# Kernel tuning notes

Hardware: AMD Instinct MI355X
Metric: run time of the kernel (lower is better)

Reference implementation:

```python
import jax, jax.numpy as jnp
from jax import lax
import numpy as np

SEQ, B, IN, H = 512, 64, 1024, 1024


def setup_inputs() -> dict:
    key = jax.random.key(0)
    ks = jax.random.split(key, 9)
    s = 0.02
    return {
        "x":   jax.random.normal(ks[0], (SEQ, B, IN), dtype=jnp.float32),
        # layer 0: Linear(input_dim, hidden) and Linear(hidden, hidden)
        "Wi0": jax.random.normal(ks[1], (H, IN), dtype=jnp.float32) * s,
        "bi0": jax.random.normal(ks[2], (H,), dtype=jnp.float32) * s,
        "Wh0": jax.random.normal(ks[3], (H, H), dtype=jnp.float32) * s,
        "bh0": jax.random.normal(ks[4], (H,), dtype=jnp.float32) * s,
        # layer 1: Linear(hidden, hidden) twice
        "Wi1": jax.random.normal(ks[5], (H, H), dtype=jnp.float32) * s,
        "bi1": jax.random.normal(ks[6], (H,), dtype=jnp.float32) * s,
        "Wh1": jax.random.normal(ks[7], (H, H), dtype=jnp.float32) * s,
        "bh1": jax.random.normal(ks[8], (H,), dtype=jnp.float32) * s,
    }


def reference(x, Wi0, bi0, Wh0, bh0, Wi1, bi1, Wh1, bh1):
    # x: [seq, batch, in]; two-layer tanh RNN, time-major, zero initial hidden.
    batch = x.shape[1]
    hdim = Wh0.shape[0]
    h0 = jnp.zeros((2, batch, hdim), dtype=x.dtype)

    def step(h_prev, x_t):
        h1 = jnp.tanh(x_t @ Wi0.T + bi0 + h_prev[0] @ Wh0.T + bh0)
        h2 = jnp.tanh(h1 @ Wi1.T + bi1 + h_prev[1] @ Wh1.T + bh1)
        return jnp.stack([h1, h2], axis=0), h2

    h_final, outputs = lax.scan(step, h0, x)
    return outputs, h_final
```

## Files before the change

### kernel.cpp

```cpp
#include <hip/hip_runtime.h>


#define SEQ 512
#define BATCH 64
#define HID 1024
#define BH (BATCH * HID)
#define DEPTH 8

typedef __attribute__((ext_vector_type(8))) short short8;
typedef __attribute__((ext_vector_type(4))) float f32x4;
typedef __attribute__((ext_vector_type(4))) unsigned int u32x4;

__device__ __forceinline__ unsigned short f32_to_bf16_rne(float f) {
    unsigned int u = __float_as_uint(f);
    u += 0x7FFFu + ((u >> 16) & 1u);
    return (unsigned short)(u >> 16);
}

__device__ __forceinline__ short8 cvt8(float4 f0, float4 f1) {
    short8 w;
    w[0] = (short)f32_to_bf16_rne(f0.x);
    w[1] = (short)f32_to_bf16_rne(f0.y);
    w[2] = (short)f32_to_bf16_rne(f0.z);
    w[3] = (short)f32_to_bf16_rne(f0.w);
    w[4] = (short)f32_to_bf16_rne(f1.x);
    w[5] = (short)f32_to_bf16_rne(f1.y);
    w[6] = (short)f32_to_bf16_rne(f1.z);
    w[7] = (short)f32_to_bf16_rne(f1.w);
    return w;
}

__device__ __forceinline__ void ld_cc16(short8& d, const unsigned short* p) {
    asm volatile("global_load_dwordx4 %0, %1, off sc0 sc1"
                 : "=v"(d) : "v"(p) : "memory");
}

__device__ __forceinline__ void vm_wait0() {
    asm volatile("s_waitcnt vmcnt(0)" ::: "memory");
    __builtin_amdgcn_sched_barrier(0);
}

__device__ __forceinline__ void st_cc16(unsigned short* p, unsigned v) {
    asm volatile("global_store_short %0, %1, off sc0 sc1"
                 :: "v"(p), "v"(v) : "memory");
}

__device__ __forceinline__ unsigned min_u16x4(u32x4 w, unsigned mn) {
    #pragma unroll
    for (int j = 0; j < 4; ++j) {
        unsigned lo = w[j] & 0xFFFFu, hi = w[j] >> 16;
        mn = mn < lo ? mn : lo;
        mn = mn < hi ? mn : hi;
    }
    return mn;
}

__device__ __forceinline__ void wait_one32(const unsigned short* f, int target) {
    if (target <= 0) return;
    for (;;) {
        u32x4 r[4];
        #pragma unroll
        for (int i = 0; i < 4; ++i)
            asm volatile("global_load_dwordx4 %0, %1, off sc0 sc1"
                         : "=v"(r[i]) : "v"((const unsigned int*)f + i * 4) : "memory");
        asm volatile("s_waitcnt vmcnt(0)" ::: "memory");
        __builtin_amdgcn_sched_barrier(0);
        unsigned mn = 0xFFFFu;
        #pragma unroll
        for (int i = 0; i < 4; ++i) mn = min_u16x4(r[i], mn);
        if ((int)mn >= target) return;
        __builtin_amdgcn_s_sleep(1);
    }
}

__device__ __forceinline__ void wait_two32(const unsigned short* f0, int t0,
                                           const unsigned short* f1, int t1) {
    if (t0 <= 0 && t1 <= 0) return;
    for (;;) {
        u32x4 r0[4], r1[4];
        #pragma unroll
        for (int i = 0; i < 4; ++i)
            asm volatile("global_load_dwordx4 %0, %1, off sc0 sc1"
                         : "=v"(r0[i]) : "v"((const unsigned int*)f0 + i * 4) : "memory");
        #pragma unroll
        for (int i = 0; i < 4; ++i)
            asm volatile("global_load_dwordx4 %0, %1, off sc0 sc1"
                         : "=v"(r1[i]) : "v"((const unsigned int*)f1 + i * 4) : "memory");
        asm volatile("s_waitcnt vmcnt(0)" ::: "memory");
        __builtin_amdgcn_sched_barrier(0);
        unsigned m0 = 0xFFFFu, m1 = 0xFFFFu;
        #pragma unroll
        for (int i = 0; i < 4; ++i) { m0 = min_u16x4(r0[i], m0); m1 = min_u16x4(r1[i], m1); }
        if ((int)m0 >= t0 && (int)m1 >= t1) return;
        __builtin_amdgcn_s_sleep(1);
    }
}

#define MFMA16(W, A, ACC) \
    ACC = __builtin_amdgcn_mfma_f32_16x16x32_bf16((W), (A), (ACC), 0, 0, 0)

__device__ __forceinline__ void ring_mm16(const unsigned short* pr, size_t aoff,
                                          const short8* wreg, f32x4& acc) {
    short8 a[16];
    #pragma unroll
    for (int k = 0; k < 16; ++k)
        ld_cc16(a[k], pr + aoff + k * 32);
    vm_wait0();
    #pragma unroll
    for (int k = 0; k < 16; ++k)
        MFMA16(wreg[k], a[k], acc);
}

__global__ void cvt_f32_bf16(const float* __restrict__ src,
                             unsigned short* __restrict__ dst, int n4) {
    int i = blockIdx.x * blockDim.x + threadIdx.x;
    int stride = gridDim.x * blockDim.x;
    for (; i < n4; i += stride) {
        float4 f = ((const float4*)src)[i];
        ushort4 o;
        o.x = f32_to_bf16_rne(f.x);
        o.y = f32_to_bf16_rne(f.y);
        o.z = f32_to_bf16_rne(f.z);
        o.w = f32_to_bf16_rne(f.w);
        ((ushort4*)dst)[i] = o;
    }
}

__global__ void init_ws(uint4* __restrict__ p, int n16) {
    int i = blockIdx.x * blockDim.x + threadIdx.x;
    if (i < n16) p[i] = make_uint4(0u, 0u, 0u, 0u);
}

__global__ __launch_bounds__(512, 1) void rnn_mfma(
    const float* __restrict__ x,
    const unsigned short* __restrict__ xb, int use_xb,
    const float* __restrict__ Wi0, const float* __restrict__ bi0,
    const float* __restrict__ Wh0, const float* __restrict__ bh0,
    const float* __restrict__ Wi1, const float* __restrict__ bi1,
    const float* __restrict__ Wh1, const float* __restrict__ bh1,
    float* __restrict__ out,
    unsigned short* __restrict__ rings,
    unsigned short* __restrict__ flags)
{
    unsigned short* h1ring = rings;
    unsigned short* h2ring = rings + DEPTH * BH;

    const int tid   = threadIdx.x;
    const int wg    = blockIdx.x;
    const int layer = wg >> 7;
    const int rg4   = (wg >> 5) & 3;
    const int nb32  = wg & 31;
    const int wv    = tid >> 6;
    const int lane  = tid & 63;
    const int fb    = wv >> 2;
    const int srcw  = (wv >> 1) & 1;
    const int kh    = wv & 1;

    unsigned short* gL0 = flags + (0 * 4 + rg4) * 64;
    unsigned short* gL1 = flags + (1 * 4 + rg4) * 64;
    unsigned short* ep_self = (layer ? gL1 : gL0) + nb32;

    const float* Wsel = layer ? (srcw ? Wh1 : Wi1) : (srcw ? Wh0 : Wi0);
    const int f_w = nb32 * 32 + fb * 16 + (lane & 15);
    const int kcb = kh * 512 + (lane >> 4) * 8;
    short8 wreg[16];
    {
        const float* rw = Wsel + (size_t)f_w * HID + kcb;
        #pragma unroll
        for (int ks = 0; ks < 16; ++ks)
            wreg[ks] = cvt8(*(const float4*)(rw + ks * 32),
                            *(const float4*)(rw + ks * 32 + 4));
    }

    const int arow = rg4 * 16 + (lane & 15);
    const size_t aoff = (size_t)arow * HID + kcb;

    const int r_feat = tid & 31;
    const int r_row  = tid >> 5;
    const int gf     = nb32 * 32 + r_feat;
    const int grow   = rg4 * 16 + r_row;
    const float* biv = layer ? bi1 : bi0;
    const float* bhv = layer ? bh1 : bh0;
    const float biasv = biv[gf] + bhv[gf];
    const int rw_base = (r_feat >> 4) * 4;

    __shared__ float red[8][16][17];

    for (int s = 0; s < SEQ; ++s) {
        f32x4 acc = {0.f, 0.f, 0.f, 0.f};

        if (layer == 0 && srcw == 0) {
            if (use_xb) {
                const unsigned short* px = xb + (size_t)s * BH + aoff;
                #pragma unroll
                for (int ks = 0; ks < 16; ++ks) {
                    short8 a = *(const short8*)(px + ks * 32);
                    MFMA16(wreg[ks], a, acc);
                }
            } else {
                const float* px = x + (size_t)s * BH + aoff;
                #pragma unroll
                for (int ks = 0; ks < 16; ++ks) {
                    short8 a = cvt8(*(const float4*)(px + ks * 32),
                                    *(const float4*)(px + ks * 32 + 4));
                    MFMA16(wreg[ks], a, acc);
                }
            }
        } else if (layer == 0) {
            if (lane == 0) wait_two32(gL0, s, gL1, s - (DEPTH - 1));
            ring_mm16(h1ring + (size_t)((s - 1) & (DEPTH - 1)) * BH, aoff, wreg, acc);
        } else if (srcw == 1) {
            if (lane == 0) wait_one32(gL1, s);
            ring_mm16(h2ring + (size_t)((s - 1) & (DEPTH - 1)) * BH, aoff, wreg, acc);
        } else {
            if (lane == 0) wait_one32(gL0, s + 1);
            ring_mm16(h1ring + (size_t)(s & (DEPTH - 1)) * BH, aoff, wreg, acc);
        }

        #pragma unroll
        for (int r = 0; r < 4; ++r)
            red[wv][4 * (lane >> 4) + r][lane & 15] = acc[r];
        __syncthreads();

        float v;
        {
            const int ff = r_feat & 15;
            v = red[rw_base][ff][r_row] + red[rw_base + 1][ff][r_row]
              + red[rw_base + 2][ff][r_row] + red[rw_base + 3][ff][r_row] + biasv;
            v = tanhf(v);
            unsigned short* ring_self =
                (layer ? h2ring : h1ring) + (size_t)(s & (DEPTH - 1)) * BH;
            st_cc16(ring_self + (size_t)grow * HID + gf, f32_to_bf16_rne(v));
        }

        asm volatile("s_waitcnt vmcnt(0)" ::: "memory");
        __builtin_amdgcn_sched_barrier(0);
        __syncthreads();
        if (tid == 0)
            st_cc16(ep_self, (unsigned)(s + 1));

        if (layer == 1) {
            out[(size_t)s * BH + (size_t)grow * HID + gf] = v;
            if (s == SEQ - 1)
                out[(size_t)SEQ * BH + BH + (size_t)grow * HID + gf] = v;
        } else if (s == SEQ - 1) {
            out[(size_t)SEQ * BH + (size_t)grow * HID + gf] = v;
        }
    }
}

extern "C" void kernel_launch(void* const* d_in, const int* in_sizes, int n_in,
                              void* d_out, int out_size, void* d_ws, size_t ws_size,
                              hipStream_t stream) {
    const float* xp   = (const float*)d_in[0];
    const float* Wi0p = (const float*)d_in[1];
    const float* bi0p = (const float*)d_in[2];
    const float* Wh0p = (const float*)d_in[3];
    const float* bh0p = (const float*)d_in[4];
    const float* Wi1p = (const float*)d_in[5];
    const float* bi1p = (const float*)d_in[6];
    const float* Wh1p = (const float*)d_in[7];
    const float* bh1p = (const float*)d_in[8];
    float* outp = (float*)d_out;

    unsigned short* rings = (unsigned short*)d_ws;
    const size_t ring_bytes = (size_t)2 * DEPTH * BH * sizeof(unsigned short);
    unsigned short* flags = (unsigned short*)((char*)d_ws + ring_bytes);
    const size_t flag_pad = 4096;
    unsigned short* xb = (unsigned short*)((char*)d_ws + ring_bytes + flag_pad);
    const size_t xb_bytes = (size_t)SEQ * BH * 2;
    const int use_xb = (ws_size >= ring_bytes + flag_pad + xb_bytes) ? 1 : 0;

    {
        const int n16 = (int)((ring_bytes + flag_pad) / 16);
        init_ws<<<(n16 + 255) / 256, 256, 0, stream>>>((uint4*)d_ws, n16);
    }
    if (use_xb)
        cvt_f32_bf16<<<2048, 256, 0, stream>>>(xp, xb, SEQ * BH / 4);

    rnn_mfma<<<dim3(256), dim3(512), 0, stream>>>(
        xp, xb, use_xb,
        Wi0p, bi0p, Wh0p, bh0p, Wi1p, bi1p, Wh1p, bh1p,
        outp, rings, flags);
}
```

Measured before the change: 3.853 ms.

## Wait only on K-half producer flags and double-buffer flag polling loads

Each wave now polls only the 16 producer flags that cover its half of the K dimension, instead of all 32 flags for the row group. This lets a wave start its ring matmul as soon as the producers it actually reads from are done. The polling loop also keeps one batch of flag loads in flight while it checks the previous batch, which shortens each spin iteration. The write-after-read guard on the layer-1 flags is narrowed to half of the consumers as well. That is a risk, because every layer-1 workgroup reads each layer-0 feature, so a ring slot could be overwritten before some reader has finished with it.

New measurement: 3.949 ms. 1.02x slower.

```diff
diff --git a/kernel.cpp b/kernel.cpp
--- a/kernel.cpp
+++ b/kernel.cpp
@@ -55,45 +55,53 @@
     return mn;
 }
 
-__device__ __forceinline__ void wait_one32(const unsigned short* f, int target) {
+__device__ __forceinline__ void issue_half(u32x4& r0, u32x4& r1,
+                                           const unsigned short* f) {
+    asm volatile("global_load_dwordx4 %0, %1, off sc0 sc1"
+                 : "=v"(r0) : "v"((const unsigned int*)f) : "memory");
+    asm volatile("global_load_dwordx4 %0, %1, off sc0 sc1"
+                 : "=v"(r1) : "v"((const unsigned int*)f + 4) : "memory");
+}
+
+__device__ __forceinline__ void wait_half(const unsigned short* f, int target) {
     if (target <= 0) return;
+    u32x4 a0, a1, b0, b1;
+    issue_half(a0, a1, f);
     for (;;) {
-        u32x4 r[4];
-        #pragma unroll
-        for (int i = 0; i < 4; ++i)
-            asm volatile("global_load_dwordx4 %0, %1, off sc0 sc1"
-                         : "=v"(r[i]) : "v"((const unsigned int*)f + i * 4) : "memory");
-        asm volatile("s_waitcnt vmcnt(0)" ::: "memory");
-        __builtin_amdgcn_sched_barrier(0);
-        unsigned mn = 0xFFFFu;
-        #pragma unroll
-        for (int i = 0; i < 4; ++i) mn = min_u16x4(r[i], mn);
-        if ((int)mn >= target) return;
-        __builtin_amdgcn_s_sleep(1);
-    }
-}
-
-__device__ __forceinline__ void wait_two32(const unsigned short* f0, int t0,
+        issue_half(b0, b1, f);
+        asm volatile("s_waitcnt vmcnt(2)" ::: "memory");
+        __builtin_amdgcn_sched_barrier(0);
+        if ((int)min_u16x4(a1, min_u16x4(a0, 0xFFFFu)) >= target) break;
+        __builtin_amdgcn_s_sleep(1);
+        issue_half(a0, a1, f);
+        asm volatile("s_waitcnt vmcnt(2)" ::: "memory");
+        __builtin_amdgcn_sched_barrier(0);
+        if ((int)min_u16x4(b1, min_u16x4(b0, 0xFFFFu)) >= target) break;
+        __builtin_amdgcn_s_sleep(1);
+    }
+    vm_wait0();
+}
+
+__device__ __forceinline__ void wait_half2(const unsigned short* f0, int t0,
                                            const unsigned short* f1, int t1) {
     if (t0 <= 0 && t1 <= 0) return;
+    u32x4 a0, a1, a2, a3, b0, b1, b2, b3;
+    issue_half(a0, a1, f0); issue_half(a2, a3, f1);
     for (;;) {
-        u32x4 r0[4], r1[4];
-        #pragma unroll
-        for (int i = 0; i < 4; ++i)
-            asm volatile("global_load_dwordx4 %0, %1, off sc0 sc1"
-                         : "=v"(r0[i]) : "v"((const unsigned int*)f0 + i * 4) : "memory");
-        #pragma unroll
-        for (int i = 0; i < 4; ++i)
-            asm volatile("global_load_dwordx4 %0, %1, off sc0 sc1"
-                         : "=v"(r1[i]) : "v"((const unsigned int*)f1 + i * 4) : "memory");
-        asm volatile("s_waitcnt vmcnt(0)" ::: "memory");
-        __builtin_amdgcn_sched_barrier(0);
-        unsigned m0 = 0xFFFFu, m1 = 0xFFFFu;
-        #pragma unroll
-        for (int i = 0; i < 4; ++i) { m0 = min_u16x4(r0[i], m0); m1 = min_u16x4(r1[i], m1); }
-        if ((int)m0 >= t0 && (int)m1 >= t1) return;
-        __builtin_amdgcn_s_sleep(1);
-    }
+        issue_half(b0, b1, f0); issue_half(b2, b3, f1);
+        asm volatile("s_waitcnt vmcnt(4)" ::: "memory");
+        __builtin_amdgcn_sched_barrier(0);
+        if ((int)min_u16x4(a1, min_u16x4(a0, 0xFFFFu)) >= t0 &&
+            (int)min_u16x4(a3, min_u16x4(a2, 0xFFFFu)) >= t1) break;
+        __builtin_amdgcn_s_sleep(1);
+        issue_half(a0, a1, f0); issue_half(a2, a3, f1);
+        asm volatile("s_waitcnt vmcnt(4)" ::: "memory");
+        __builtin_amdgcn_sched_barrier(0);
+        if ((int)min_u16x4(b1, min_u16x4(b0, 0xFFFFu)) >= t0 &&
+            (int)min_u16x4(b3, min_u16x4(b2, 0xFFFFu)) >= t1) break;
+        __builtin_amdgcn_s_sleep(1);
+    }
+    vm_wait0();
 }
 
 #define MFMA16(W, A, ACC) \
@@ -159,6 +167,8 @@
     unsigned short* gL0 = flags + (0 * 4 + rg4) * 64;
     unsigned short* gL1 = flags + (1 * 4 + rg4) * 64;
     unsigned short* ep_self = (layer ? gL1 : gL0) + nb32;
+    const unsigned short* dataL0 = gL0 + kh * 16;
+    const unsigned short* dataL1 = gL1 + kh * 16;
 
     const float* Wsel = layer ? (srcw ? Wh1 : Wi1) : (srcw ? Wh0 : Wi0);
     const int f_w = nb32 * 32 + fb * 16 + (lane & 15);
@@ -207,13 +217,13 @@
                 }
             }
         } else if (layer == 0) {
-            if (lane == 0) wait_two32(gL0, s, gL1, s - (DEPTH - 1));
+            if (lane == 0) wait_half2(dataL0, s, dataL1, s - (DEPTH - 1));
             ring_mm16(h1ring + (size_t)((s - 1) & (DEPTH - 1)) * BH, aoff, wreg, acc);
         } else if (srcw == 1) {
-            if (lane == 0) wait_one32(gL1, s);
+            if (lane == 0) wait_half(dataL1, s);
             ring_mm16(h2ring + (size_t)((s - 1) & (DEPTH - 1)) * BH, aoff, wreg, acc);
         } else {
-            if (lane == 0) wait_one32(gL0, s + 1);
+            if (lane == 0) wait_half(dataL0, s + 1);
             ring_mm16(h1ring + (size_t)(s & (DEPTH - 1)) * BH, aoff, wreg, acc);
         }
 
```

## Tag ring entries with step counter to replace flag polling with data polling

Applied to the files above, without the earlier changes.

Each hidden-state ring entry is widened to 32 bits and carries the bf16 value plus the producing step number. Consumers poll the data itself until every tag matches, so the per-step flag round trip before reading is gone. The flag is now written right after the reduction barrier and serves only as ring-slot backpressure. Ring depth drops to 4, and a double-buffered shared reduction array removes the second barrier. The cost is twice the ring traffic, the tag-check work on each poll, and correctness now relies on each 32-bit store being seen atomically.

Result: slower. 11.46 ms (+197.5%).

```diff
diff --git a/kernel.cpp b/kernel.cpp
--- a/kernel.cpp
+++ b/kernel.cpp
@@ -5,7 +5,7 @@
 #define BATCH 64
 #define HID 1024
 #define BH (BATCH * HID)
-#define DEPTH 8
+#define DEPTH 4
 
 typedef __attribute__((ext_vector_type(8))) short short8;
 typedef __attribute__((ext_vector_type(4))) float f32x4;
@@ -30,16 +30,15 @@
     return w;
 }
 
-__device__ __forceinline__ void ld_cc16(short8& d, const unsigned short* p) {
-    asm volatile("global_load_dwordx4 %0, %1, off sc0 sc1"
-                 : "=v"(d) : "v"(p) : "memory");
-}
-
 __device__ __forceinline__ void vm_wait0() {
     asm volatile("s_waitcnt vmcnt(0)" ::: "memory");
     __builtin_amdgcn_sched_barrier(0);
 }
 
+__device__ __forceinline__ void st_cc32(unsigned* p, unsigned v) {
+    asm volatile("global_store_dword %0, %1, off sc0 sc1"
+                 :: "v"(p), "v"(v) : "memory");
+}
 __device__ __forceinline__ void st_cc16(unsigned short* p, unsigned v) {
     asm volatile("global_store_short %0, %1, off sc0 sc1"
                  :: "v"(p), "v"(v) : "memory");
@@ -55,7 +54,7 @@
     return mn;
 }
 
-__device__ __forceinline__ void wait_one32(const unsigned short* f, int target) {
+__device__ __forceinline__ void wait_grp32(const unsigned short* f, int target) {
     if (target <= 0) return;
     for (;;) {
         u32x4 r[4];
@@ -73,42 +72,50 @@
     }
 }
 
-__device__ __forceinline__ void wait_two32(const unsigned short* f0, int t0,
-                                           const unsigned short* f1, int t1) {
-    if (t0 <= 0 && t1 <= 0) return;
-    for (;;) {
-        u32x4 r0[4], r1[4];
-        #pragma unroll
-        for (int i = 0; i < 4; ++i)
-            asm volatile("global_load_dwordx4 %0, %1, off sc0 sc1"
-                         : "=v"(r0[i]) : "v"((const unsigned int*)f0 + i * 4) : "memory");
-        #pragma unroll
-        for (int i = 0; i < 4; ++i)
-            asm volatile("global_load_dwordx4 %0, %1, off sc0 sc1"
-                         : "=v"(r1[i]) : "v"((const unsigned int*)f1 + i * 4) : "memory");
-        asm volatile("s_waitcnt vmcnt(0)" ::: "memory");
-        __builtin_amdgcn_sched_barrier(0);
-        unsigned m0 = 0xFFFFu, m1 = 0xFFFFu;
-        #pragma unroll
-        for (int i = 0; i < 4; ++i) { m0 = min_u16x4(r0[i], m0); m1 = min_u16x4(r1[i], m1); }
-        if ((int)m0 >= t0 && (int)m1 >= t1) return;
-        __builtin_amdgcn_s_sleep(1);
-    }
-}
-
 #define MFMA16(W, A, ACC) \
     ACC = __builtin_amdgcn_mfma_f32_16x16x32_bf16((W), (A), (ACC), 0, 0, 0)
 
-__device__ __forceinline__ void ring_mm16(const unsigned short* pr, size_t aoff,
-                                          const short8* wreg, f32x4& acc) {
-    short8 a[16];
-    #pragma unroll
-    for (int k = 0; k < 16; ++k)
-        ld_cc16(a[k], pr + aoff + k * 32);
+__device__ __forceinline__ bool try_ring_mm(const unsigned* pr, unsigned tag,
+                                            const short8* wreg, f32x4& accio) {
+    u32x4 lo[16], hi[16];
+    #pragma unroll
+    for (int ks = 0; ks < 16; ++ks) {
+        const unsigned* p = pr + ks * 32;
+        asm volatile("global_load_dwordx4 %0, %1, off sc0 sc1"
+                     : "=v"(lo[ks]) : "v"(p) : "memory");
+        asm volatile("global_load_dwordx4 %0, %1, off sc0 sc1"
+                     : "=v"(hi[ks]) : "v"(p + 4) : "memory");
+    }
     vm_wait0();
-    #pragma unroll
-    for (int k = 0; k < 16; ++k)
-        MFMA16(wreg[k], a[k], acc);
+    unsigned d = 0;
+    #pragma unroll
+    for (int ks = 0; ks < 16; ++ks) {
+        #pragma unroll
+        for (int j = 0; j < 4; ++j) {
+            d |= lo[ks][j] ^ tag;
+            d |= hi[ks][j] ^ tag;
+        }
+    }
+    if (!__all((d & 0xFFFFu) == 0u)) return false;
+    f32x4 acc = accio;
+    #pragma unroll
+    for (int ks = 0; ks < 16; ++ks) {
+        u32x4 pk;
+        pk[0] = (lo[ks][0] >> 16) | (lo[ks][1] & 0xFFFF0000u);
+        pk[1] = (lo[ks][2] >> 16) | (lo[ks][3] & 0xFFFF0000u);
+        pk[2] = (hi[ks][0] >> 16) | (hi[ks][1] & 0xFFFF0000u);
+        pk[3] = (hi[ks][2] >> 16) | (hi[ks][3] & 0xFFFF0000u);
+        short8 a = __builtin_bit_cast(short8, pk);
+        MFMA16(wreg[ks], a, acc);
+    }
+    accio = acc;
+    return true;
+}
+
+__device__ __forceinline__ void ring_mm_poll(const unsigned* pr, unsigned tag,
+                                             const short8* wreg, f32x4& acc) {
+    while (!try_ring_mm(pr, tag, wreg, acc))
+        __builtin_amdgcn_s_sleep(1);
 }
 
 __global__ void cvt_f32_bf16(const float* __restrict__ src,
@@ -139,11 +146,11 @@
     const float* __restrict__ Wi1, const float* __restrict__ bi1,
     const float* __restrict__ Wh1, const float* __restrict__ bh1,
     float* __restrict__ out,
-    unsigned short* __restrict__ rings,
+    unsigned* __restrict__ rings32,
     unsigned short* __restrict__ flags)
 {
-    unsigned short* h1ring = rings;
-    unsigned short* h2ring = rings + DEPTH * BH;
+    unsigned* h1r = rings32;
+    unsigned* h2r = rings32 + DEPTH * BH;
 
     const int tid   = threadIdx.x;
     const int wg    = blockIdx.x;
@@ -184,10 +191,20 @@
     const float biasv = biv[gf] + bhv[gf];
     const int rw_base = (r_feat >> 4) * 4;
 
-    __shared__ float red[8][16][17];
+    __shared__ float red[2][8][16][17];
 
     for (int s = 0; s < SEQ; ++s) {
+        const int par = s & 1;
         f32x4 acc = {0.f, 0.f, 0.f, 0.f};
+
+        if (tid == 0) {
+            if (layer == 0) {
+                wait_grp32(gL0, s - (DEPTH - 2));
+                wait_grp32(gL1, s - (DEPTH - 1));
+            } else {
+                wait_grp32(gL1, s - (DEPTH - 2));
+            }
+        }
 
         if (layer == 0 && srcw == 0) {
             if (use_xb) {
@@ -207,44 +224,41 @@
                 }
             }
         } else if (layer == 0) {
-            if (lane == 0) wait_two32(gL0, s, gL1, s - (DEPTH - 1));
-            ring_mm16(h1ring + (size_t)((s - 1) & (DEPTH - 1)) * BH, aoff, wreg, acc);
+            ring_mm_poll(h1r + (size_t)((s - 1) & (DEPTH - 1)) * BH + aoff,
+                         (unsigned)s, wreg, acc);
         } else if (srcw == 1) {
-            if (lane == 0) wait_one32(gL1, s);
-            ring_mm16(h2ring + (size_t)((s - 1) & (DEPTH - 1)) * BH, aoff, wreg, acc);
+            ring_mm_poll(h2r + (size_t)((s - 1) & (DEPTH - 1)) * BH + aoff,
+                         (unsigned)s, wreg, acc);
         } else {
-            if (lane == 0) wait_one32(gL0, s + 1);
-            ring_mm16(h1ring + (size_t)(s & (DEPTH - 1)) * BH, aoff, wreg, acc);
+            ring_mm_poll(h1r + (size_t)(s & (DEPTH - 1)) * BH + aoff,
+                         (unsigned)(s + 1), wreg, acc);
         }
 
         #pragma unroll
         for (int r = 0; r < 4; ++r)
-            red[wv][4 * (lane >> 4) + r][lane & 15] = acc[r];
+            red[par][wv][4 * (lane >> 4) + r][lane & 15] = acc[r];
         __syncthreads();
 
-        float v;
+        if (tid == 0)
+            st_cc16(ep_self, (unsigned)(s + 1));
+
         {
             const int ff = r_feat & 15;
-            v = red[rw_base][ff][r_row] + red[rw_base + 1][ff][r_row]
-              + red[rw_base + 2][ff][r_row] + red[rw_base + 3][ff][r_row] + biasv;
+            float v = red[par][rw_base][ff][r_row] + red[par][rw_base + 1][ff][r_row]
+                    + red[par][rw_base + 2][ff][r_row] + red[par][rw_base + 3][ff][r_row]
+                    + biasv;
             v = tanhf(v);
-            unsigned short* ring_self =
-                (layer ? h2ring : h1ring) + (size_t)(s & (DEPTH - 1)) * BH;
-            st_cc16(ring_self + (size_t)grow * HID + gf, f32_to_bf16_rne(v));
-        }
-
-        asm volatile("s_waitcnt vmcnt(0)" ::: "memory");
-        __builtin_amdgcn_sched_barrier(0);
-        __syncthreads();
-        if (tid == 0)
-            st_cc16(ep_self, (unsigned)(s + 1));
-
-        if (layer == 1) {
-            out[(size_t)s * BH + (size_t)grow * HID + gf] = v;
-            if (s == SEQ - 1)
-                out[(size_t)SEQ * BH + BH + (size_t)grow * HID + gf] = v;
-        } else if (s == SEQ - 1) {
-            out[(size_t)SEQ * BH + (size_t)grow * HID + gf] = v;
+            unsigned tagged = ((unsigned)f32_to_bf16_rne(v) << 16) | (unsigned)(s + 1);
+            unsigned* ring_self = (layer ? h2r : h1r) + (size_t)(s & (DEPTH - 1)) * BH;
+            st_cc32(ring_self + (size_t)grow * HID + gf, tagged);
+
+            if (layer == 1) {
+                out[(size_t)s * BH + (size_t)grow * HID + gf] = v;
+                if (s == SEQ - 1)
+                    out[(size_t)SEQ * BH + BH + (size_t)grow * HID + gf] = v;
+            } else if (s == SEQ - 1) {
+                out[(size_t)SEQ * BH + (size_t)grow * HID + gf] = v;
+            }
         }
     }
 }
@@ -263,8 +277,8 @@
     const float* bh1p = (const float*)d_in[8];
     float* outp = (float*)d_out;
 
-    unsigned short* rings = (unsigned short*)d_ws;
-    const size_t ring_bytes = (size_t)2 * DEPTH * BH * sizeof(unsigned short);
+    unsigned* rings32 = (unsigned*)d_ws;
+    const size_t ring_bytes = (size_t)2 * DEPTH * BH * sizeof(unsigned);
     unsigned short* flags = (unsigned short*)((char*)d_ws + ring_bytes);
     const size_t flag_pad = 4096;
     unsigned short* xb = (unsigned short*)((char*)d_ws + ring_bytes + flag_pad);
@@ -281,5 +295,5 @@
     rnn_mfma<<<dim3(256), dim3(512), 0, stream>>>(
         xp, xb, use_xb,
         Wi0p, bi0p, Wh0p, bh0p, Wi1p, bi1p, Wh1p, bh1p,
-        outp, rings, flags);
-}
+        outp, rings32, flags);
+}
```

## Replace block barriers with per-wave LDS flag handoff and finer global flags

Applied to the files above, without the earlier changes.

Removes both __syncthreads per timestep. Each 16-feature half of the block now reduces independently: three producer waves post partial sums to double-buffered LDS and signal with workgroup-scope atomics, and a fourth wave adds its own partial, applies bias and tanh, writes four packed bf16 values, and publishes a per-half global flag. The global flag array doubles to 64 entries per row group, so consumers poll twice as many flags, and all waves (not only lane 0) now spin on them. This is meant to cut intra-block barrier stalls and let halves progress independently, at the cost of more polling traffic and more complex spin-based synchronization.

Result: slower. 10.34 ms (+168.5%).

```diff
diff --git a/kernel.cpp b/kernel.cpp
--- a/kernel.cpp
+++ b/kernel.cpp
@@ -44,6 +44,17 @@
     asm volatile("global_store_short %0, %1, off sc0 sc1"
                  :: "v"(p), "v"(v) : "memory");
 }
+__device__ __forceinline__ void st_cc64(unsigned short* p, unsigned long long v) {
+    asm volatile("global_store_dwordx2 %0, %1, off sc0 sc1"
+                 :: "v"(p), "v"(v) : "memory");
+}
+
+__device__ __forceinline__ unsigned long long pack4_bf16(float a, float b, float c, float d) {
+    return (unsigned long long)f32_to_bf16_rne(a)
+         | ((unsigned long long)f32_to_bf16_rne(b) << 16)
+         | ((unsigned long long)f32_to_bf16_rne(c) << 32)
+         | ((unsigned long long)f32_to_bf16_rne(d) << 48);
+}
 
 __device__ __forceinline__ unsigned min_u16x4(u32x4 w, unsigned mn) {
     #pragma unroll
@@ -55,42 +66,42 @@
     return mn;
 }
 
-__device__ __forceinline__ void wait_one32(const unsigned short* f, int target) {
+__device__ __forceinline__ void wait_one64(const unsigned short* f, int target) {
     if (target <= 0) return;
     for (;;) {
-        u32x4 r[4];
-        #pragma unroll
-        for (int i = 0; i < 4; ++i)
+        u32x4 r[8];
+        #pragma unroll
+        for (int i = 0; i < 8; ++i)
             asm volatile("global_load_dwordx4 %0, %1, off sc0 sc1"
                          : "=v"(r[i]) : "v"((const unsigned int*)f + i * 4) : "memory");
         asm volatile("s_waitcnt vmcnt(0)" ::: "memory");
         __builtin_amdgcn_sched_barrier(0);
         unsigned mn = 0xFFFFu;
         #pragma unroll
-        for (int i = 0; i < 4; ++i) mn = min_u16x4(r[i], mn);
+        for (int i = 0; i < 8; ++i) mn = min_u16x4(r[i], mn);
         if ((int)mn >= target) return;
         __builtin_amdgcn_s_sleep(1);
     }
 }
 
-__device__ __forceinline__ void wait_two32(const unsigned short* f0, int t0,
+__device__ __forceinline__ void wait_two64(const unsigned short* f0, int t0,
                                            const unsigned short* f1, int t1) {
     if (t0 <= 0 && t1 <= 0) return;
     for (;;) {
-        u32x4 r0[4], r1[4];
-        #pragma unroll
-        for (int i = 0; i < 4; ++i)
+        u32x4 r0[8], r1[8];
+        #pragma unroll
+        for (int i = 0; i < 8; ++i)
             asm volatile("global_load_dwordx4 %0, %1, off sc0 sc1"
                          : "=v"(r0[i]) : "v"((const unsigned int*)f0 + i * 4) : "memory");
         #pragma unroll
-        for (int i = 0; i < 4; ++i)
+        for (int i = 0; i < 8; ++i)
             asm volatile("global_load_dwordx4 %0, %1, off sc0 sc1"
                          : "=v"(r1[i]) : "v"((const unsigned int*)f1 + i * 4) : "memory");
         asm volatile("s_waitcnt vmcnt(0)" ::: "memory");
         __builtin_amdgcn_sched_barrier(0);
         unsigned m0 = 0xFFFFu, m1 = 0xFFFFu;
         #pragma unroll
-        for (int i = 0; i < 4; ++i) { m0 = min_u16x4(r0[i], m0); m1 = min_u16x4(r1[i], m1); }
+        for (int i = 0; i < 8; ++i) { m0 = min_u16x4(r0[i], m0); m1 = min_u16x4(r1[i], m1); }
         if ((int)m0 >= t0 && (int)m1 >= t1) return;
         __builtin_amdgcn_s_sleep(1);
     }
@@ -153,14 +164,14 @@
     const int wv    = tid >> 6;
     const int lane  = tid & 63;
     const int fb    = wv >> 2;
-    const int srcw  = (wv >> 1) & 1;
-    const int kh    = wv & 1;
+    const int r2    = wv & 3;
+    const int kh    = r2 & 1;
 
     unsigned short* gL0 = flags + (0 * 4 + rg4) * 64;
     unsigned short* gL1 = flags + (1 * 4 + rg4) * 64;
-    unsigned short* ep_self = (layer ? gL1 : gL0) + nb32;
-
-    const float* Wsel = layer ? (srcw ? Wh1 : Wi1) : (srcw ? Wh0 : Wi0);
+    unsigned short* ep_self = (layer ? gL1 : gL0) + nb32 * 2 + fb;
+
+    const float* Wsel = layer ? (r2 < 2 ? Wh1 : Wi1) : (r2 < 2 ? Wi0 : Wh0);
     const int f_w = nb32 * 32 + fb * 16 + (lane & 15);
     const int kcb = kh * 512 + (lane >> 4) * 8;
     short8 wreg[16];
@@ -175,21 +186,30 @@
     const int arow = rg4 * 16 + (lane & 15);
     const size_t aoff = (size_t)arow * HID + kcb;
 
-    const int r_feat = tid & 31;
-    const int r_row  = tid >> 5;
-    const int gf     = nb32 * 32 + r_feat;
-    const int grow   = rg4 * 16 + r_row;
+    const int f0   = nb32 * 32 + fb * 16 + 4 * (lane >> 4);
+    const int grow = rg4 * 16 + (lane & 15);
     const float* biv = layer ? bi1 : bi0;
     const float* bhv = layer ? bh1 : bh0;
-    const float biasv = biv[gf] + bhv[gf];
-    const int rw_base = (r_feat >> 4) * 4;
-
-    __shared__ float red[8][16][17];
+    float bias4[4];
+    #pragma unroll
+    for (int r = 0; r < 4; ++r) bias4[r] = biv[f0 + r] + bhv[f0 + r];
+
+    __shared__ float part[2][2][3][16][17];
+    __shared__ unsigned post[2][3];
+    __shared__ unsigned done_[2];
+
+    if (tid == 0) {
+        post[0][0] = post[0][1] = post[0][2] = 0u;
+        post[1][0] = post[1][1] = post[1][2] = 0u;
+        done_[0] = done_[1] = 0u;
+    }
+    __syncthreads();
 
     for (int s = 0; s < SEQ; ++s) {
+        const int par = s & 1;
         f32x4 acc = {0.f, 0.f, 0.f, 0.f};
 
-        if (layer == 0 && srcw == 0) {
+        if (layer == 0 && r2 < 2) {
             if (use_xb) {
                 const unsigned short* px = xb + (size_t)s * BH + aoff;
                 #pragma unroll
@@ -207,44 +227,67 @@
                 }
             }
         } else if (layer == 0) {
-            if (lane == 0) wait_two32(gL0, s, gL1, s - (DEPTH - 1));
+            if (r2 == 3) wait_two64(gL0, s, gL1, s - (DEPTH - 1));
+            else         wait_one64(gL0, s);
             ring_mm16(h1ring + (size_t)((s - 1) & (DEPTH - 1)) * BH, aoff, wreg, acc);
-        } else if (srcw == 1) {
-            if (lane == 0) wait_one32(gL1, s);
+        } else if (r2 < 2) {
+            wait_one64(gL1, s);
             ring_mm16(h2ring + (size_t)((s - 1) & (DEPTH - 1)) * BH, aoff, wreg, acc);
         } else {
-            if (lane == 0) wait_one32(gL0, s + 1);
+            wait_one64(gL0, s + 1);
             ring_mm16(h1ring + (size_t)(s & (DEPTH - 1)) * BH, aoff, wreg, acc);
         }
 
-        #pragma unroll
-        for (int r = 0; r < 4; ++r)
-            red[wv][4 * (lane >> 4) + r][lane & 15] = acc[r];
-        __syncthreads();
-
-        float v;
-        {
-            const int ff = r_feat & 15;
-            v = red[rw_base][ff][r_row] + red[rw_base + 1][ff][r_row]
-              + red[rw_base + 2][ff][r_row] + red[rw_base + 3][ff][r_row] + biasv;
-            v = tanhf(v);
+        if (r2 != 3) {
+            while ((int)__hip_atomic_load(&done_[fb], __ATOMIC_ACQUIRE,
+                                          __HIP_MEMORY_SCOPE_WORKGROUP) < s - 1)
+                __builtin_amdgcn_s_sleep(0);
+            #pragma unroll
+            for (int r = 0; r < 4; ++r)
+                part[par][fb][r2][4 * (lane >> 4) + r][lane & 15] = acc[r];
+            if (lane == 0)
+                __hip_atomic_store(&post[fb][r2], (unsigned)(s + 1),
+                                   __ATOMIC_RELEASE, __HIP_MEMORY_SCOPE_WORKGROUP);
+        } else {
+            const unsigned need = (unsigned)(s + 1);
+            for (;;) {
+                unsigned p0 = __hip_atomic_load(&post[fb][0], __ATOMIC_ACQUIRE,
+                                                __HIP_MEMORY_SCOPE_WORKGROUP);
+                unsigned p1 = __hip_atomic_load(&post[fb][1], __ATOMIC_ACQUIRE,
+                                                __HIP_MEMORY_SCOPE_WORKGROUP);
+                unsigned p2 = __hip_atomic_load(&post[fb][2], __ATOMIC_ACQUIRE,
+                                                __HIP_MEMORY_SCOPE_WORKGROUP);
+                if (p0 >= need && p1 >= need && p2 >= need) break;
+                __builtin_amdgcn_s_sleep(0);
+            }
+            #pragma unroll
+            for (int r = 0; r < 4; ++r) {
+                const int ff = 4 * (lane >> 4) + r;
+                acc[r] += part[par][fb][0][ff][lane & 15]
+                        + part[par][fb][1][ff][lane & 15]
+                        + part[par][fb][2][ff][lane & 15] + bias4[r];
+            }
+            if (lane == 0)
+                __hip_atomic_store(&done_[fb], (unsigned)(s + 1), __ATOMIC_RELEASE,
+                                   __HIP_MEMORY_SCOPE_WORKGROUP);
+            float v0 = tanhf(acc[0]), v1 = tanhf(acc[1]);
+            float v2 = tanhf(acc[2]), v3 = tanhf(acc[3]);
             unsigned short* ring_self =
                 (layer ? h2ring : h1ring) + (size_t)(s & (DEPTH - 1)) * BH;
-            st_cc16(ring_self + (size_t)grow * HID + gf, f32_to_bf16_rne(v));
-        }
-
-        asm volatile("s_waitcnt vmcnt(0)" ::: "memory");
-        __builtin_amdgcn_sched_barrier(0);
-        __syncthreads();
-        if (tid == 0)
-            st_cc16(ep_self, (unsigned)(s + 1));
-
-        if (layer == 1) {
-            out[(size_t)s * BH + (size_t)grow * HID + gf] = v;
-            if (s == SEQ - 1)
-                out[(size_t)SEQ * BH + BH + (size_t)grow * HID + gf] = v;
-        } else if (s == SEQ - 1) {
-            out[(size_t)SEQ * BH + (size_t)grow * HID + gf] = v;
+            st_cc64(ring_self + (size_t)grow * HID + f0, pack4_bf16(v0, v1, v2, v3));
+            vm_wait0();
+            if (lane == 0)
+                st_cc16(ep_self, (unsigned)(s + 1));
+            if (layer == 1) {
+                *(float4*)(out + (size_t)s * BH + (size_t)grow * HID + f0) =
+                    make_float4(v0, v1, v2, v3);
+                if (s == SEQ - 1)
+                    *(float4*)(out + (size_t)SEQ * BH + BH + (size_t)grow * HID + f0) =
+                        make_float4(v0, v1, v2, v3);
+            } else if (s == SEQ - 1) {
+                *(float4*)(out + (size_t)SEQ * BH + (size_t)grow * HID + f0) =
+                    make_float4(v0, v1, v2, v3);
+            }
         }
     }
 }
```
